# Kernel tuning notes

Hardware: AMD Instinct MI355X
Metric: run time of the kernel (lower is better)

## Reference

```python
import jax, jax.numpy as jnp
import numpy as np
from jax import lax

DIM = 180; NH = 6; WH = 16; WW = 16; MH = 8; MW = 8
HD = DIM // (2 * NH)  # 15, head dim; also the (non-sqrt) scale
RMS_EPS = 1.1920929e-07  # torch.finfo(float32).eps (RMSNorm eps=None)

def _conv(x, w, b, pad):
    # x: NHWC, w: HWIO
    return lax.conv_general_dilated(x, w, (1, 1), [(pad, pad), (pad, pad)],
                                    dimension_numbers=('NHWC', 'HWIO', 'NHWC')) + b

def _lrelu(x):
    return jnp.where(x >= 0, x, 0.2 * x)

def _ln(x, w, b, eps=1e-5):
    m = x.mean(-1, keepdims=True)
    v = jnp.mean((x - m) ** 2, -1, keepdims=True)
    return (x - m) / jnp.sqrt(v + eps) * w + b

def _forward(x, dfe_w1, dfe_b1, dfe_w2, dfe_b2, dfe_w3, dfe_b3, dfe_lw, dfe_lb,
             sl_w, sl_b, pos_pw, pos_pb, ln1w, ln1b, l1w, l1b, ln2w, ln2b,
             l2w, l2b, ln3w, ln3b, l3w, l3b, proj_w, proj_b, norm_w):
    B, C, H, W = x.shape
    xh = jnp.transpose(x, (0, 2, 3, 1))  # NHWC
    shortcut = xh
    # DFE: conv branch gated by 1x1 linear branch
    h = _lrelu(_conv(xh, dfe_w1, dfe_b1, 0))
    h = _lrelu(_conv(h, dfe_w2, dfe_b2, 1))
    h = _conv(h, dfe_w3, dfe_b3, 0)
    qv = h * _conv(xh, dfe_lw, dfe_lb, 0)  # (B,H,W,C)
    # window partition
    L = WH * WW
    qv = qv.reshape(B, H // WH, WH, W // WW, WW, C).transpose(0, 1, 3, 2, 4, 5).reshape(-1, L, C)
    Bw = qv.shape[0]
    qv = qv.reshape(Bw, L, 2, NH, HD).transpose(2, 0, 3, 1, 4)
    q, v = qv[0], qv[1]  # (Bw, NH, L, HD)
    # spatial linear projection of v: downsample window -> base window
    rH, rW = WH // MH, WW // MW
    vp = v.reshape(Bw, NH, MH, rH, MW, rW, HD).transpose(0, 1, 2, 4, 6, 3, 5)
    vp = vp.reshape(Bw, NH, MH * MW, HD, rH * rW)
    vp = ((vp @ sl_w) + sl_b)[..., 0]  # (Bw, NH, mapL, HD)
    corr = jnp.einsum('bhlc,bhmc->bhlm', q, vp) / HD  # (Bw, NH, L, mapL)
    # dynamic relative position bias
    bh = jnp.arange(1 - WH, WH, dtype=jnp.float32)
    bw = jnp.arange(1 - WW, WW, dtype=jnp.float32)
    biases = jnp.stack(jnp.meshgrid(bh, bw, indexing='ij')).reshape(2, -1).T  # (nb, 2)
    p = biases @ pos_pw + pos_pb
    p = jax.nn.relu(_ln(p, ln1w, ln1b)) @ l1w + l1b
    p = jax.nn.relu(_ln(p, ln2w, ln2b)) @ l2w + l2b
    pos = jax.nn.relu(_ln(p, ln3w, ln3b)) @ l3w + l3b  # (nb, NH)
    coords = jnp.stack(jnp.meshgrid(jnp.arange(WH), jnp.arange(WW), indexing='ij')).reshape(2, -1)
    rel = coords[:, :, None] - coords[:, None, :]  # (2, L, L)
    idx = (rel[0] + WH - 1) * (2 * WW - 1) + (rel[1] + WW - 1)  # (L, L)
    rpb = pos[idx.reshape(-1)].reshape(L, MH, rH, MW, rW, NH)
    rpb = rpb.transpose(0, 1, 3, 5, 2, 4).reshape(L, MH * MW, NH, rH * rW).mean(-1)
    rpb = rpb.transpose(2, 0, 1)  # (NH, L, mapL)
    corr = corr + rpb[None]
    xs = jnp.einsum('bhlm,bhmc->bhlc', corr, vp).transpose(0, 2, 1, 3).reshape(Bw, L, NH * HD)
    # channel self-correlation
    qc = q.transpose(0, 2, 1, 3).reshape(Bw, L, NH * HD)
    vc = v.transpose(0, 2, 1, 3).reshape(Bw, L, NH * HD)
    cmap = jnp.einsum('blc,bld->bcd', qc, vc) / L  # (Bw, C/2, C/2)
    xc = jnp.einsum('bcd,bld->blc', cmap, vc)  # (Bw, L, C/2)
    # window reverse
    def wrev(win):
        c = win.shape[-1]
        return win.reshape(B, H // WH, W // WW, WH, WW, c).transpose(0, 1, 3, 2, 4, 5).reshape(B, H, W, c)
    xs = wrev(xs.reshape(Bw, WH, WW, NH * HD))
    xc = wrev(xc.reshape(Bw, WH, WW, NH * HD))
    y = jnp.concatenate([xs, xc], -1)  # (B, H, W, C)
    y = y @ proj_w + proj_b
    y = y * (1.0 / jnp.sqrt(jnp.mean(y * y, -1, keepdims=True) + RMS_EPS)) * norm_w
    y = shortcut + y
    return jnp.transpose(y, (0, 3, 1, 2))


def setup_inputs() -> dict:
    key = jax.random.key(0)
    ks = iter(jax.random.split(key, 32))
    def rn(shape, s=0.05):
        return jax.random.normal(next(ks), shape, jnp.float32) * s
    inp = {}
    inp['x'] = jax.random.normal(next(ks), (4, 180, 256, 256), jnp.float32)
    inp['dfe_w1'] = rn((1, 1, 180, 36)); inp['dfe_b1'] = rn((36,))
    inp['dfe_w2'] = rn((3, 3, 36, 36)); inp['dfe_b2'] = rn((36,))
    inp['dfe_w3'] = rn((1, 1, 36, 180)); inp['dfe_b3'] = rn((180,))
    inp['dfe_lw'] = rn((1, 1, 180, 180)); inp['dfe_lb'] = rn((180,))
    inp['sl_w'] = rn((4, 1)); inp['sl_b'] = rn((1,))
    inp['pos_pw'] = rn((2, 11)); inp['pos_pb'] = rn((11,))
    inp['ln1w'] = jnp.ones((11,)); inp['ln1b'] = jnp.zeros((11,))
    inp['l1w'] = rn((11, 11)); inp['l1b'] = rn((11,))
    inp['ln2w'] = jnp.ones((11,)); inp['ln2b'] = jnp.zeros((11,))
    inp['l2w'] = rn((11, 11)); inp['l2b'] = rn((11,))
    inp['ln3w'] = jnp.ones((11,)); inp['ln3b'] = jnp.zeros((11,))
    inp['l3w'] = rn((11, 6)); inp['l3b'] = rn((6,))
    inp['proj_w'] = rn((180, 180)); inp['proj_b'] = rn((180,))
    inp['norm_w'] = jnp.ones((180,))
    return inp


def reference(x, dfe_w1, dfe_b1, dfe_w2, dfe_b2, dfe_w3, dfe_b3, dfe_lw, dfe_lb,
              sl_w, sl_b, pos_pw, pos_pb, ln1w, ln1b, l1w, l1b, ln2w, ln2b,
              l2w, l2b, ln3w, ln3b, l3w, l3b, proj_w, proj_b, norm_w):
    return _forward(x, dfe_w1, dfe_b1, dfe_w2, dfe_b2, dfe_w3, dfe_b3, dfe_lw, dfe_lb,
                    sl_w, sl_b, pos_pw, pos_pb, ln1w, ln1b, l1w, l1b, ln2w, ln2b,
                    l2w, l2b, ln3w, ln3b, l3w, l3b, proj_w, proj_b, norm_w)
```

## Files before the change

kernel.cpp:

```cpp
#include <hip/hip_runtime.h>
#include <stdint.h>

typedef unsigned short u16;
typedef unsigned int   u32;

#define HW 65536

typedef __bf16 bf16x8 __attribute__((ext_vector_type(8)));
typedef float  f32x4  __attribute__((ext_vector_type(4)));

static __device__ __forceinline__ float bf2f(u16 h) {
    u32 u = ((u32)h) << 16;
    return __builtin_bit_cast(float, u);
}
static __device__ __forceinline__ u16 f2bf(float f) {
    u32 u = __builtin_bit_cast(u32, f);
    u += 0x7fffu + ((u >> 16) & 1u);
    return (u16)(u >> 16);
}
static __device__ __forceinline__ void bf2x2(u32 u, float& a, float& b) {
    a = __builtin_bit_cast(float, u << 16);
    b = __builtin_bit_cast(float, u & 0xffff0000u);
}
static __device__ __forceinline__ f32x4 mfma16(bf16x8 a, bf16x8 b, f32x4 c) {
    return __builtin_amdgcn_mfma_f32_16x16x32_bf16(a, b, c, 0, 0, 0);
}

static __device__ __forceinline__ void lnrelu11(float* p, const float* __restrict__ w,
                                                const float* __restrict__ b) {
    float m = 0.f;
    #pragma unroll
    for (int k = 0; k < 11; k++) m += p[k];
    m *= (1.0f / 11.0f);
    float v = 0.f;
    #pragma unroll
    for (int k = 0; k < 11; k++) { float d = p[k] - m; v = fmaf(d, d, v); }
    v *= (1.0f / 11.0f);
    float r = 1.0f / sqrtf(v + 1e-5f);
    #pragma unroll
    for (int k = 0; k < 11; k++) {
        float t = (p[k] - m) * r * w[k] + b[k];
        p[k] = t > 0.f ? t : 0.f;
    }
}

__global__ __launch_bounds__(1024) void k_pos(
    const float* __restrict__ pw, const float* __restrict__ pb,
    const float* __restrict__ ln1w, const float* __restrict__ ln1b,
    const float* __restrict__ l1w, const float* __restrict__ l1b,
    const float* __restrict__ ln2w, const float* __restrict__ ln2b,
    const float* __restrict__ l2w, const float* __restrict__ l2b,
    const float* __restrict__ ln3w, const float* __restrict__ ln3b,
    const float* __restrict__ l3w, const float* __restrict__ l3b,
    float* __restrict__ pos)
{
    int i = threadIdx.x;
    if (i >= 961) return;
    float b0 = (float)(i / 31) - 15.0f;
    float b1 = (float)(i % 31) - 15.0f;
    float p[11], t[11];
    #pragma unroll
    for (int j = 0; j < 11; j++) p[j] = b0 * pw[j] + b1 * pw[11 + j] + pb[j];
    lnrelu11(p, ln1w, ln1b);
    #pragma unroll
    for (int j = 0; j < 11; j++) {
        float s = l1b[j];
        #pragma unroll
        for (int k = 0; k < 11; k++) s = fmaf(p[k], l1w[k * 11 + j], s);
        t[j] = s;
    }
    lnrelu11(t, ln2w, ln2b);
    #pragma unroll
    for (int j = 0; j < 11; j++) {
        float s = l2b[j];
        #pragma unroll
        for (int k = 0; k < 11; k++) s = fmaf(t[k], l2w[k * 11 + j], s);
        p[j] = s;
    }
    lnrelu11(p, ln3w, ln3b);
    #pragma unroll
    for (int h = 0; h < 6; h++) {
        float s = l3b[h];
        #pragma unroll
        for (int k = 0; k < 11; k++) s = fmaf(p[k], l3w[k * 6 + h], s);
        pos[i * 6 + h] = s;
    }
}

__global__ __launch_bounds__(256) void k_rpb(const float* __restrict__ pos,
                                             float* __restrict__ rpb)
{
    int g = blockIdx.x * 256 + threadIdx.x;
    if (g >= 6 * 256 * 64) return;
    int h = g >> 14;
    int l = (g >> 6) & 255;
    int m = g & 63;
    int yl = l >> 4, xl = l & 15;
    int my = m >> 3, mx = m & 7;
    float s = 0.f;
    #pragma unroll
    for (int ry = 0; ry < 2; ry++) {
        #pragma unroll
        for (int rx = 0; rx < 2; rx++) {
            int y2 = my * 2 + ry, x2 = mx * 2 + rx;
            int idx = (yl - y2 + 15) * 31 + (xl - x2 + 15);
            s += pos[idx * 6 + h];
        }
    }
    rpb[g] = 0.25f * s;
}

__global__ __launch_bounds__(256) void k_conv1(const float* __restrict__ x,
                                               const float* __restrict__ w,
                                               const float* __restrict__ b,
                                               u16* __restrict__ h1)
{
    int pix = blockIdx.x * 256 + threadIdx.x;
    int bb = pix >> 16, sp = pix & 65535;
    float acc[36];
    #pragma unroll
    for (int j = 0; j < 36; j++) acc[j] = b[j];
    const float* xp = x + (size_t)bb * 180 * HW + sp;
    for (int c = 0; c < 180; c++) {
        float xv = xp[(size_t)c * HW];
        #pragma unroll
        for (int j = 0; j < 36; j++) acc[j] = fmaf(xv, w[c * 36 + j], acc[j]);
    }
    u16* hp = h1 + (size_t)bb * 36 * HW + sp;
    #pragma unroll
    for (int j = 0; j < 36; j++) {
        float v = acc[j];
        v = v >= 0.f ? v : 0.2f * v;
        hp[(size_t)j * HW] = f2bf(v);
    }
}

__global__ __launch_bounds__(256) void k_conv3(const u16* __restrict__ h1,
                                               const float* __restrict__ w,
                                               const float* __restrict__ b,
                                               u16* __restrict__ h2)
{
    int tx = threadIdx.x, ty = threadIdx.y;
    int x0 = blockIdx.x * 16 + tx;
    int y0 = blockIdx.y * 16 + ty;
    int bb = blockIdx.z;
    float acc[36];
    #pragma unroll
    for (int j = 0; j < 36; j++) acc[j] = b[j];
    const u16* base = h1 + (size_t)bb * 36 * HW;
    for (int ky = 0; ky < 3; ky++) {
        int yy = y0 + ky - 1;
        if (yy < 0 || yy >= 256) continue;
        for (int kx = 0; kx < 3; kx++) {
            int xx = x0 + kx - 1;
            if (xx < 0 || xx >= 256) continue;
            const u16* ip = base + yy * 256 + xx;
            const float* wp = w + ((ky * 3 + kx) * 36) * 36;
            for (int c = 0; c < 36; c++) {
                float v = bf2f(ip[(size_t)c * HW]);
                #pragma unroll
                for (int j = 0; j < 36; j++) acc[j] = fmaf(v, wp[c * 36 + j], acc[j]);
            }
        }
    }
    u16* op = h2 + (size_t)bb * 36 * HW + y0 * 256 + x0;
    #pragma unroll
    for (int j = 0; j < 36; j++) {
        float v = acc[j];
        v = v >= 0.f ? v : 0.2f * v;
        op[(size_t)j * HW] = f2bf(v);
    }
}

__global__ __launch_bounds__(256) void k_gate(const u16* __restrict__ h2,
                                              const float* __restrict__ x,
                                              const float* __restrict__ w3,
                                              const float* __restrict__ b3,
                                              const float* __restrict__ lw,
                                              const float* __restrict__ lb,
                                              u16* __restrict__ qvT)
{
    int lane = threadIdx.x;
    int g = __builtin_amdgcn_readfirstlane((int)threadIdx.y);
    int cb = g * 45;
    int blk = blockIdx.x;
    int bb = blk >> 10;
    int r  = blk & 1023;
    int wx = r & 15;
    int yq = r >> 4;
    int yl = lane >> 4, xl = lane & 15;
    int y  = yq * 4 + yl;
    int sp = y * 256 + wx * 16 + xl;
    int w  = bb * 256 + (yq >> 2) * 16 + wx;
    int l  = ((yq & 3) * 4 + yl) * 16 + xl;

    float ah[45], al[45];
    #pragma unroll
    for (int j = 0; j < 45; j++) { ah[j] = b3[cb + j]; al[j] = lb[cb + j]; }
    const u16* hp = h2 + (size_t)bb * 36 * HW + sp;
    for (int c = 0; c < 36; c++) {
        float hv = bf2f(hp[(size_t)c * HW]);
        #pragma unroll
        for (int j = 0; j < 45; j++) ah[j] = fmaf(hv, w3[c * 180 + cb + j], ah[j]);
    }
    const float* xp = x + (size_t)bb * 180 * HW + sp;
    for (int c = 0; c < 180; c++) {
        float xv = xp[(size_t)c * HW];
        #pragma unroll
        for (int j = 0; j < 45; j++) al[j] = fmaf(xv, lw[c * 180 + cb + j], al[j]);
    }
    u16* qp = qvT + (size_t)w * 180 * 256 + l;
    #pragma unroll
    for (int j = 0; j < 45; j++) qp[(size_t)(cb + j) * 256] = f2bf(ah[j] * al[j]);
}

__global__ __launch_bounds__(256) void k_spat(const u16* __restrict__ qvT,
                                              const float* __restrict__ rpb,
                                              const float* __restrict__ slw,
                                              const float* __restrict__ slb,
                                              u16* __restrict__ yp)
{
    __shared__ __align__(16) float vp[6144];
    int w = blockIdx.x;
    int bb = w >> 8, wy = (w >> 4) & 15, wx = w & 15;
    int t = threadIdx.x;
    int lane = t & 63, wv = t >> 6;
    const u16* qw = qvT + (size_t)w * 180 * 256;
    float s0 = slw[0], s1 = slw[1], s2 = slw[2], s3 = slw[3], sb = slb[0];
    for (int o = t; o < 384; o += 256) vp[(o >> 6) * 1024 + (o & 63) * 16 + 15] = 0.f;
    for (int it = 0; it < 23; it++) {
        int p = wv + it * 4;
        if (p < 90) {
            int mm = lane;
            int l0 = (mm >> 3) * 32 + (mm & 7) * 2;
            const u16* rp2 = qw + (size_t)(90 + p) * 256;
            float s = sb + s0 * bf2f(rp2[l0]) + s1 * bf2f(rp2[l0 + 1])
                         + s2 * bf2f(rp2[l0 + 16]) + s3 * bf2f(rp2[l0 + 17]);
            vp[(p / 15) * 1024 + mm * 16 + (p % 15)] = s;
        }
    }
    __syncthreads();
    int l = t;
    size_t pixl = (size_t)((bb * 256 + wy * 16 + (l >> 4)) * 256 + wx * 16 + (l & 15));
    u16* op = yp + pixl * 192;
    ((u32*)op)[45] = 0u; ((u32*)op)[46] = 0u; ((u32*)op)[47] = 0u;
    for (int h = 0; h < 6; h++) {
        float q[16];
        #pragma unroll
        for (int d = 0; d < 15; d++) q[d] = bf2f(qw[(size_t)(h * 15 + d) * 256 + l]);
        q[15] = 0.f;
        float acc[16];
        #pragma unroll
        for (int d = 0; d < 16; d++) acc[d] = 0.f;
        const float* rp = rpb + ((h * 256 + l) << 6);
        const float4* vph = (const float4*)(vp + (h << 10));
        for (int m0 = 0; m0 < 64; m0 += 4) {
            float ra[4];
            *(float4*)ra = *(const float4*)(rp + m0);
            #pragma unroll
            for (int mm = 0; mm < 4; mm++) {
                int m = m0 + mm;
                float wvv[16];
                ((float4*)wvv)[0] = vph[m * 4 + 0];
                ((float4*)wvv)[1] = vph[m * 4 + 1];
                ((float4*)wvv)[2] = vph[m * 4 + 2];
                ((float4*)wvv)[3] = vph[m * 4 + 3];
                float s = 0.f;
                #pragma unroll
                for (int d2 = 0; d2 < 16; d2++) s = fmaf(q[d2], wvv[d2], s);
                s = s * (1.0f / 15.0f) + ra[mm];
                #pragma unroll
                for (int d2 = 0; d2 < 16; d2++) acc[d2] = fmaf(s, wvv[d2], acc[d2]);
            }
        }
        #pragma unroll
        for (int d = 0; d < 15; d++) op[h * 15 + d] = f2bf(acc[d]);
    }
}

__global__ __launch_bounds__(256) void k_chan(const u16* __restrict__ qvT,
                                              u16* __restrict__ yp)
{
    __shared__ __align__(16) u16 cm[96 * 104];
    __shared__ __align__(16) u16 xcb[128 * 104];
    int w = blockIdx.x;
    int bb = w >> 8, wy = (w >> 4) & 15, wx = w & 15;
    int t = threadIdx.x;
    int lane = t & 63, wv = t >> 6;
    int m = lane & 15, quad = lane >> 4;
    const u16* qw = qvT + (size_t)w * 180 * 256;

    int ct0 = (wv & 1) * 3, dt0 = (wv >> 1) * 3;
    f32x4 acc[3][3];
    #pragma unroll
    for (int i = 0; i < 3; i++)
        #pragma unroll
        for (int j = 0; j < 3; j++) {
            f32x4 z = {0.f, 0.f, 0.f, 0.f};
            acc[i][j] = z;
        }
    #pragma unroll
    for (int ks = 0; ks < 8; ks++) {
        bf16x8 A[3], B[3];
        #pragma unroll
        for (int i = 0; i < 3; i++)
            A[i] = *(const bf16x8*)(qw + (size_t)((ct0 + i) * 16 + m) * 256 + ks * 32 + quad * 8);
        #pragma unroll
        for (int j = 0; j < 3; j++) {
            int d = (dt0 + j) * 16 + m;
            int dd = d > 89 ? 89 : d;
            B[j] = *(const bf16x8*)(qw + (size_t)(90 + dd) * 256 + ks * 32 + quad * 8);
        }
        #pragma unroll
        for (int i = 0; i < 3; i++)
            #pragma unroll
            for (int j = 0; j < 3; j++)
                acc[i][j] = mfma16(A[i], B[j], acc[i][j]);
    }
    #pragma unroll
    for (int i = 0; i < 3; i++)
        #pragma unroll
        for (int j = 0; j < 3; j++)
            #pragma unroll
            for (int r = 0; r < 4; r++)
                cm[((ct0 + i) * 16 + quad * 4 + r) * 104 + (dt0 + j) * 16 + m] =
                    f2bf(acc[i][j][r] * (1.0f / 256.0f));
    __syncthreads();
    if (t < 96) {
        u32* z = (u32*)(cm + t * 104 + 90);
        z[0] = 0; z[1] = 0; z[2] = 0;
    }
    __syncthreads();

    int base_pix = (bb * 256 + wy * 16) * 256 + wx * 16;
    const __bf16* qwb = (const __bf16*)qw;
    for (int half = 0; half < 2; half++) {
        #pragma unroll
        for (int i = 0; i < 2; i++) {
            int ltl = wv * 2 + i;
            int lt = half * 8 + ltl;
            bf16x8 A[3];
            #pragma unroll
            for (int ks = 0; ks < 3; ks++) {
                const __bf16* colp = qwb + lt * 16 + m;
                #pragma unroll
                for (int j2 = 0; j2 < 8; j2++) {
                    int d = ks * 32 + quad * 8 + j2;
                    int dd = d > 89 ? 89 : d;
                    A[ks][j2] = colp[(size_t)(90 + dd) * 256];
                }
            }
            for (int ct = 0; ct < 6; ct++) {
                f32x4 c4 = {0.f, 0.f, 0.f, 0.f};
                #pragma unroll
                for (int ks = 0; ks < 3; ks++) {
                    bf16x8 B = *(const bf16x8*)(cm + (ct * 16 + m) * 104 + ks * 32 + quad * 8);
                    c4 = mfma16(A[ks], B, c4);
                }
                #pragma unroll
                for (int r = 0; r < 4; r++)
                    xcb[(ltl * 16 + quad * 4 + r) * 104 + ct * 16 + m] = f2bf(c4[r]);
            }
        }
        __syncthreads();
        #pragma unroll
        for (int it = 0; it < 6; it++) {
            int gg = t + it * 256;
            int lrow = gg / 12, seg = gg % 12;
            int l = half * 128 + lrow;
            int pix = base_pix + (l >> 4) * 256 + (l & 15);
            *(uint4*)(yp + (size_t)pix * 192 + 96 + seg * 8) =
                *(const uint4*)(xcb + lrow * 104 + seg * 8);
        }
        __syncthreads();
    }
}

__global__ __launch_bounds__(256) void k_wprep(const float* __restrict__ pjw,
                                               u16* __restrict__ whiT,
                                               u16* __restrict__ wloT)
{
    int g = blockIdx.x * 256 + threadIdx.x;
    int oc = g / 192, k = g % 192;
    int kp = -1;
    if (k < 90) kp = k;
    else if (k >= 96 && k < 186) kp = k - 6;
    float v = (kp >= 0 && oc < 180) ? pjw[kp * 180 + oc] : 0.f;
    u16 h = f2bf(v);
    float lo = v - bf2f(h);
    whiT[g] = h;
    wloT[g] = f2bf(lo);
}

__global__ __launch_bounds__(256) void k_proj(const u16* __restrict__ yp,
                                              const float* __restrict__ x,
                                              const u16* __restrict__ whiT,
                                              const u16* __restrict__ wloT,
                                              const float* __restrict__ pb,
                                              const float* __restrict__ nw,
                                              float* __restrict__ out)
{
    __shared__ float part[4][4][16];
    int t = threadIdx.x;
    int lane = t & 63;
    int g = __builtin_amdgcn_readfirstlane(t >> 6);
    int m = lane & 15, q = lane >> 4;
    int pix0 = blockIdx.x * 64;
    int ocbase = g * 48;

    f32x4 acc[3][4];
    #pragma unroll
    for (int mt = 0; mt < 3; mt++)
        #pragma unroll
        for (int pt = 0; pt < 4; pt++) {
            f32x4 z = {0.f, 0.f, 0.f, 0.f};
            acc[mt][pt] = z;
        }

    const u16* bbase = yp + (size_t)pix0 * 192;
    #pragma unroll 2
    for (int ks = 0; ks < 6; ks++) {
        bf16x8 B[4];
        #pragma unroll
        for (int pt = 0; pt < 4; pt++)
            B[pt] = *(const bf16x8*)(bbase + (size_t)(pt * 16 + m) * 192 + ks * 32 + q * 8);
        #pragma unroll
        for (int mt = 0; mt < 3; mt++) {
            bf16x8 Ah = *(const bf16x8*)(whiT + (size_t)(ocbase + mt * 16 + m) * 192 + ks * 32 + q * 8);
            bf16x8 Al = *(const bf16x8*)(wloT + (size_t)(ocbase + mt * 16 + m) * 192 + ks * 32 + q * 8);
            #pragma unroll
            for (int pt = 0; pt < 4; pt++) {
                acc[mt][pt] = mfma16(Ah, B[pt], acc[mt][pt]);
                acc[mt][pt] = mfma16(Al, B[pt], acc[mt][pt]);
            }
        }
    }

    float pbv[3][4], nwv[3][4];
    #pragma unroll
    for (int mt = 0; mt < 3; mt++)
        #pragma unroll
        for (int r = 0; r < 4; r++) {
            int oc = ocbase + mt * 16 + q * 4 + r;
            bool ok = oc < 180;
            pbv[mt][r] = ok ? pb[oc] : 0.f;
            nwv[mt][r] = ok ? nw[oc] : 0.f;
        }
    float ss[4] = {0.f, 0.f, 0.f, 0.f};
    #pragma unroll
    for (int mt = 0; mt < 3; mt++)
        #pragma unroll
        for (int pt = 0; pt < 4; pt++)
            #pragma unroll
            for (int r = 0; r < 4; r++) {
                float y = acc[mt][pt][r] + pbv[mt][r];
                acc[mt][pt][r] = y;
                ss[pt] = fmaf(y, y, ss[pt]);
            }
    #pragma unroll
    for (int pt = 0; pt < 4; pt++) {
        ss[pt] += __shfl_xor(ss[pt], 16);
        ss[pt] += __shfl_xor(ss[pt], 32);
    }
    if (q == 0) {
        #pragma unroll
        for (int pt = 0; pt < 4; pt++) part[g][pt][m] = ss[pt];
    }
    __syncthreads();
    float scale[4];
    #pragma unroll
    for (int pt = 0; pt < 4; pt++) {
        float tot = part[0][pt][m] + part[1][pt][m] + part[2][pt][m] + part[3][pt][m];
        scale[pt] = 1.0f / sqrtf(tot * (1.0f / 180.0f) + 1.1920929e-7f);
    }

    int bb = pix0 >> 16, sp0 = pix0 & 65535;
    const float* xb = x + (size_t)bb * 180 * HW + sp0 + m;
    float* ob = out + (size_t)bb * 180 * HW + sp0 + m;
    #pragma unroll
    for (int mt = 0; mt < 3; mt++)
        #pragma unroll
        for (int r = 0; r < 4; r++) {
            int oc = ocbase + mt * 16 + q * 4 + r;
            if (oc < 180) {
                #pragma unroll
                for (int pt = 0; pt < 4; pt++) {
                    size_t off = (size_t)oc * HW + pt * 16;
                    ob[off] = xb[off] + acc[mt][pt][r] * scale[pt] * nwv[mt][r];
                }
            }
        }
}

extern "C" void kernel_launch(void* const* d_in, const int* in_sizes, int n_in,
                              void* d_out, int out_size, void* d_ws, size_t ws_size,
                              hipStream_t stream)
{
    const float* x    = (const float*)d_in[0];
    const float* w1   = (const float*)d_in[1];
    const float* b1   = (const float*)d_in[2];
    const float* w2   = (const float*)d_in[3];
    const float* b2   = (const float*)d_in[4];
    const float* w3   = (const float*)d_in[5];
    const float* b3   = (const float*)d_in[6];
    const float* lw   = (const float*)d_in[7];
    const float* lb   = (const float*)d_in[8];
    const float* slw  = (const float*)d_in[9];
    const float* slb  = (const float*)d_in[10];
    const float* pw   = (const float*)d_in[11];
    const float* pb   = (const float*)d_in[12];
    const float* ln1w = (const float*)d_in[13];
    const float* ln1b = (const float*)d_in[14];
    const float* l1w  = (const float*)d_in[15];
    const float* l1b  = (const float*)d_in[16];
    const float* ln2w = (const float*)d_in[17];
    const float* ln2b = (const float*)d_in[18];
    const float* l2w  = (const float*)d_in[19];
    const float* l2b  = (const float*)d_in[20];
    const float* ln3w = (const float*)d_in[21];
    const float* ln3b = (const float*)d_in[22];
    const float* l3w  = (const float*)d_in[23];
    const float* l3b  = (const float*)d_in[24];
    const float* pjw  = (const float*)d_in[25];
    const float* pjb  = (const float*)d_in[26];
    const float* nw   = (const float*)d_in[27];
    float* out = (float*)d_out;

    char* ws = (char*)d_ws;
    float* pos = (float*)(ws + 0);
    float* rpb = (float*)(ws + 24576);
    u16*  h2  = (u16*)(ws + 417792);
    u16*  whiT = (u16*)(ws + 417792);
    u16*  wloT = (u16*)(ws + 417792 + 73728);
    u16*  h1  = (u16*)(ws + 19292160);
    u16*  qvT = (u16*)(ws + 19292160);
    u16*  yp  = (u16*)(ws + 113664000);

    k_pos<<<dim3(1), dim3(1024), 0, stream>>>(pw, pb, ln1w, ln1b, l1w, l1b,
                                              ln2w, ln2b, l2w, l2b, ln3w, ln3b,
                                              l3w, l3b, pos);
    k_rpb<<<dim3(384), dim3(256), 0, stream>>>(pos, rpb);
    k_conv1<<<dim3(1024), dim3(256), 0, stream>>>(x, w1, b1, h1);
    k_conv3<<<dim3(16, 16, 4), dim3(16, 16), 0, stream>>>(h1, w2, b2, h2);
    k_gate<<<dim3(4096), dim3(64, 4), 0, stream>>>(h2, x, w3, b3, lw, lb, qvT);
    k_wprep<<<dim3(144), dim3(256), 0, stream>>>(pjw, whiT, wloT);
    k_spat<<<dim3(1024), dim3(256), 0, stream>>>(qvT, rpb, slw, slb, yp);
    k_chan<<<dim3(1024), dim3(256), 0, stream>>>(qvT, yp);
    k_proj<<<dim3(4096), dim3(256), 0, stream>>>(yp, x, whiT, wloT, pjb, nw, out);
}
```

Before: 1.281 ms.

## Move gating 1x1 convs onto bf16 MFMA with hi/lo split weights

The gate kernel previously computed the two 1x1 convolutions (180->180 linear branch and 36->180 conv3) as scalar FMAs per pixel. It now runs them as bf16 MFMA matrix multiplies. Weights are pre-split into hi/lo bf16 parts by a new prep kernel, and activations are also split (three MFMAs per tile) to keep near-fp32 accuracy. This trades extra MFMA issue and a small prep launch for removing a large scalar FMA workload. The prep buffers are placed in workspace that yp later overwrites.

```diff
diff --git a/kernel.cpp b/kernel.cpp
--- a/kernel.cpp
+++ b/kernel.cpp
@@ -172,46 +172,138 @@
     }
 }
 
+__global__ __launch_bounds__(256) void k_wgprep(const float* __restrict__ lw,
+                                                const float* __restrict__ w3,
+                                                u16* __restrict__ gwh,
+                                                u16* __restrict__ gwl,
+                                                u16* __restrict__ cwh,
+                                                u16* __restrict__ cwl)
+{
+    int gidx = blockIdx.x * 256 + threadIdx.x;
+    if (gidx < 36864) {
+        int oc = gidx / 192, k = gidx % 192;
+        float v = (oc < 180 && k < 180) ? lw[k * 180 + oc] : 0.f;
+        u16 h = f2bf(v);
+        float lo = v - bf2f(h);
+        gwh[gidx] = h;
+        gwl[gidx] = f2bf(lo);
+    } else {
+        int r = gidx - 36864;
+        int oc = r / 64, k = r % 64;
+        float v = (oc < 180 && k < 36) ? w3[k * 180 + oc] : 0.f;
+        u16 h = f2bf(v);
+        float lo = v - bf2f(h);
+        cwh[r] = h;
+        cwl[r] = f2bf(lo);
+    }
+}
+
 __global__ __launch_bounds__(256) void k_gate(const u16* __restrict__ h2,
                                               const float* __restrict__ x,
-                                              const float* __restrict__ w3,
+                                              const u16* __restrict__ gwh,
+                                              const u16* __restrict__ gwl,
+                                              const u16* __restrict__ cwh,
+                                              const u16* __restrict__ cwl,
                                               const float* __restrict__ b3,
-                                              const float* __restrict__ lw,
                                               const float* __restrict__ lb,
                                               u16* __restrict__ qvT)
 {
-    int lane = threadIdx.x;
-    int g = __builtin_amdgcn_readfirstlane((int)threadIdx.y);
-    int cb = g * 45;
+    int t = threadIdx.x;
+    int lane = t & 63;
+    int g = __builtin_amdgcn_readfirstlane(t >> 6);
+    int m = lane & 15, q = lane >> 4;
     int blk = blockIdx.x;
-    int bb = blk >> 10;
-    int r  = blk & 1023;
-    int wx = r & 15;
-    int yq = r >> 4;
-    int yl = lane >> 4, xl = lane & 15;
-    int y  = yq * 4 + yl;
-    int sp = y * 256 + wx * 16 + xl;
-    int w  = bb * 256 + (yq >> 2) * 16 + wx;
-    int l  = ((yq & 3) * 4 + yl) * 16 + xl;
-
-    float ah[45], al[45];
-    #pragma unroll
-    for (int j = 0; j < 45; j++) { ah[j] = b3[cb + j]; al[j] = lb[cb + j]; }
-    const u16* hp = h2 + (size_t)bb * 36 * HW + sp;
-    for (int c = 0; c < 36; c++) {
-        float hv = bf2f(hp[(size_t)c * HW]);
-        #pragma unroll
-        for (int j = 0; j < 45; j++) ah[j] = fmaf(hv, w3[c * 180 + cb + j], ah[j]);
-    }
-    const float* xp = x + (size_t)bb * 180 * HW + sp;
-    for (int c = 0; c < 180; c++) {
-        float xv = xp[(size_t)c * HW];
-        #pragma unroll
-        for (int j = 0; j < 45; j++) al[j] = fmaf(xv, lw[c * 180 + cb + j], al[j]);
-    }
-    u16* qp = qvT + (size_t)w * 180 * 256 + l;
-    #pragma unroll
-    for (int j = 0; j < 45; j++) qp[(size_t)(cb + j) * 256] = f2bf(ah[j] * al[j]);
+    int w  = blk >> 2;
+    int lq = blk & 3;
+    int bb = w >> 8, wy = (w >> 4) & 15, wx = w & 15;
+    int ocb = g * 48;
+    int sp0 = (wy * 16 + lq * 4) * 256 + wx * 16 + m;
+    const float* xb = x + (size_t)bb * 180 * HW;
+    const u16*  hb = h2 + (size_t)bb * 36 * HW;
+
+    f32x4 accG[3][4], accC[3][4];
+    #pragma unroll
+    for (int mt = 0; mt < 3; mt++)
+        #pragma unroll
+        for (int pt = 0; pt < 4; pt++) {
+            f32x4 z = {0.f, 0.f, 0.f, 0.f};
+            accG[mt][pt] = z;
+            accC[mt][pt] = z;
+        }
+
+    #pragma unroll 2
+    for (int ks = 0; ks < 6; ks++) {
+        float xv[4][8];
+        #pragma unroll
+        for (int pt = 0; pt < 4; pt++)
+            #pragma unroll
+            for (int j = 0; j < 8; j++) {
+                int c = ks * 32 + q * 8 + j;
+                if (c > 179) c = 179;
+                xv[pt][j] = xb[(size_t)c * HW + sp0 + pt * 256];
+            }
+        bf16x8 Bh[4], Bl[4];
+        #pragma unroll
+        for (int pt = 0; pt < 4; pt++)
+            #pragma unroll
+            for (int j = 0; j < 8; j++) {
+                float v = xv[pt][j];
+                __bf16 hi = (__bf16)v;
+                Bh[pt][j] = hi;
+                Bl[pt][j] = (__bf16)(v - (float)hi);
+            }
+        #pragma unroll
+        for (int mt = 0; mt < 3; mt++) {
+            bf16x8 Ah = *(const bf16x8*)(gwh + (size_t)(ocb + mt * 16 + m) * 192 + ks * 32 + q * 8);
+            bf16x8 Al = *(const bf16x8*)(gwl + (size_t)(ocb + mt * 16 + m) * 192 + ks * 32 + q * 8);
+            #pragma unroll
+            for (int pt = 0; pt < 4; pt++) {
+                accG[mt][pt] = mfma16(Ah, Bh[pt], accG[mt][pt]);
+                accG[mt][pt] = mfma16(Al, Bh[pt], accG[mt][pt]);
+                accG[mt][pt] = mfma16(Ah, Bl[pt], accG[mt][pt]);
+            }
+        }
+    }
+
+    #pragma unroll
+    for (int ks = 0; ks < 2; ks++) {
+        bf16x8 B[4];
+        #pragma unroll
+        for (int pt = 0; pt < 4; pt++)
+            #pragma unroll
+            for (int j = 0; j < 8; j++) {
+                int c = ks * 32 + q * 8 + j;
+                if (c > 35) c = 35;
+                B[pt][j] = __builtin_bit_cast(__bf16, hb[(size_t)c * HW + sp0 + pt * 256]);
+            }
+        #pragma unroll
+        for (int mt = 0; mt < 3; mt++) {
+            bf16x8 Ah = *(const bf16x8*)(cwh + (size_t)(ocb + mt * 16 + m) * 64 + ks * 32 + q * 8);
+            bf16x8 Al = *(const bf16x8*)(cwl + (size_t)(ocb + mt * 16 + m) * 64 + ks * 32 + q * 8);
+            #pragma unroll
+            for (int pt = 0; pt < 4; pt++) {
+                accC[mt][pt] = mfma16(Ah, B[pt], accC[mt][pt]);
+                accC[mt][pt] = mfma16(Al, B[pt], accC[mt][pt]);
+            }
+        }
+    }
+
+    u16* qw = qvT + (size_t)w * 180 * 256 + lq * 64 + m;
+    #pragma unroll
+    for (int mt = 0; mt < 3; mt++)
+        #pragma unroll
+        for (int r = 0; r < 4; r++) {
+            int oc = ocb + mt * 16 + q * 4 + r;
+            if (oc < 180) {
+                float bc = b3[oc], bg = lb[oc];
+                #pragma unroll
+                for (int pt = 0; pt < 4; pt++) {
+                    float ah = accC[mt][pt][r] + bc;
+                    float al = accG[mt][pt][r] + bg;
+                    qw[(size_t)oc * 256 + pt * 16] = f2bf(ah * al);
+                }
+            }
+        }
 }
 
 __global__ __launch_bounds__(256) void k_spat(const u16* __restrict__ qvT,
@@ -535,14 +627,20 @@
     u16*  h1  = (u16*)(ws + 19292160);
     u16*  qvT = (u16*)(ws + 19292160);
     u16*  yp  = (u16*)(ws + 113664000);
-
+    u16*  gwh = (u16*)(ws + 113664000);
+    u16*  gwl = (u16*)(ws + 113664000 + 73728);
+    u16*  cwh = (u16*)(ws + 113664000 + 147456);
+    u16*  cwl = (u16*)(ws + 113664000 + 172032);
+
+    k_wgprep<<<dim3(192), dim3(256), 0, stream>>>(lw, w3, gwh, gwl, cwh, cwl);
     k_pos<<<dim3(1), dim3(1024), 0, stream>>>(pw, pb, ln1w, ln1b, l1w, l1b,
                                               ln2w, ln2b, l2w, l2b, ln3w, ln3b,
                                               l3w, l3b, pos);
     k_rpb<<<dim3(384), dim3(256), 0, stream>>>(pos, rpb);
     k_conv1<<<dim3(1024), dim3(256), 0, stream>>>(x, w1, b1, h1);
     k_conv3<<<dim3(16, 16, 4), dim3(16, 16), 0, stream>>>(h1, w2, b2, h2);
-    k_gate<<<dim3(4096), dim3(64, 4), 0, stream>>>(h2, x, w3, b3, lw, lb, qvT);
+    k_gate<<<dim3(4096), dim3(256), 0, stream>>>(h2, x, gwh, gwl, cwh, cwl,
+                                                 b3, lb, qvT);
     k_wprep<<<dim3(144), dim3(256), 0, stream>>>(pjw, whiT, wloT);
     k_spat<<<dim3(1024), dim3(256), 0, stream>>>(qvT, rpb, slw, slb, yp);
     k_chan<<<dim3(1024), dim3(256), 0, stream>>>(qvT, yp);
```

Measured after the change: 1.089 ms. -15.0%, faster.
